# Performance work log

Hardware: AMD Instinct MI355X
Metric: run time of the kernel (lower is better)

Reference implementation:

```python
import jax, jax.numpy as jnp
import numpy as np

NUM_CLASSES = 91
W_CLASS, W_BBOX, W_GIOU = 1.0, 5.0, 2.0


def cxcywh_to_xyxy(b):
    return jnp.concatenate([b[..., :2] - 0.5 * b[..., 2:], b[..., :2] + 0.5 * b[..., 2:]], axis=-1)


def pairwise_giou(b1, b2):
    # b1: [B,Q,4] xyxy, b2: [B,G,4] xyxy -> [B,Q,G]
    area1 = (b1[..., 2] - b1[..., 0]) * (b1[..., 3] - b1[..., 1])
    area2 = (b2[..., 2] - b2[..., 0]) * (b2[..., 3] - b2[..., 1])
    lt = jnp.maximum(b1[:, :, None, :2], b2[:, None, :, :2])
    rb = jnp.minimum(b1[:, :, None, 2:], b2[:, None, :, 2:])
    wh = jnp.clip(rb - lt, 0.0)
    inter = wh[..., 0] * wh[..., 1]
    union = area1[:, :, None] + area2[:, None, :] - inter
    iou = inter / union
    lt2 = jnp.minimum(b1[:, :, None, :2], b2[:, None, :, :2])
    rb2 = jnp.maximum(b1[:, :, None, 2:], b2[:, None, :, 2:])
    wh2 = jnp.clip(rb2 - lt2, 0.0)
    area_c = wh2[..., 0] * wh2[..., 1]
    return iou - (area_c - union) / area_c


def elem_giou(b1, b2):
    # b1, b2: [M,4] xyxy -> [M]
    area1 = (b1[:, 2] - b1[:, 0]) * (b1[:, 3] - b1[:, 1])
    area2 = (b2[:, 2] - b2[:, 0]) * (b2[:, 3] - b2[:, 1])
    lt = jnp.maximum(b1[:, :2], b2[:, :2])
    rb = jnp.minimum(b1[:, 2:], b2[:, 2:])
    wh = jnp.clip(rb - lt, 0.0)
    inter = wh[:, 0] * wh[:, 1]
    union = area1 + area2 - inter
    iou = inter / union
    lt2 = jnp.minimum(b1[:, :2], b2[:, :2])
    rb2 = jnp.maximum(b1[:, 2:], b2[:, 2:])
    wh2 = jnp.clip(rb2 - lt2, 0.0)
    area_c = wh2[:, 0] * wh2[:, 1]
    return iou - (area_c - union) / area_c


def _lsa(cost):
    # Rectangular linear sum assignment (scipy-style shortest augmenting path).
    cost = np.asarray(cost, dtype=np.float64)
    transposed = cost.shape[0] > cost.shape[1]
    if transposed:
        cost = cost.T
    n, m = cost.shape
    u = np.zeros(n)
    v = np.zeros(m)
    path = np.full(m, -1, dtype=np.int64)
    col4row = np.full(n, -1, dtype=np.int64)
    row4col = np.full(m, -1, dtype=np.int64)
    for cur_row in range(n):
        min_val = 0.0
        i = cur_row
        remaining = np.arange(m)
        SR = np.zeros(n, dtype=bool)
        SC = np.zeros(m, dtype=bool)
        shortest = np.full(m, np.inf)
        sink = -1
        while sink == -1:
            SR[i] = True
            r = min_val + cost[i, remaining] - u[i] - v[remaining]
            better = r < shortest[remaining]
            upd = remaining[better]
            shortest[upd] = r[better]
            path[upd] = i
            k = int(np.argmin(shortest[remaining]))
            j = int(remaining[k])
            min_val = shortest[j]
            if not np.isfinite(min_val):
                raise ValueError('infeasible cost matrix')
            if row4col[j] == -1:
                sink = j
            else:
                i = int(row4col[j])
            SC[j] = True
            remaining = np.delete(remaining, k)
        u[cur_row] += min_val
        sr = SR.copy()
        sr[cur_row] = False
        u[sr] += min_val - shortest[col4row[sr]]
        v[SC] -= min_val - shortest[SC]
        j = sink
        while True:
            i = int(path[j])
            row4col[j] = i
            col4row[i], j = j, col4row[i]
            if i == cur_row:
                break
    if transposed:
        a = np.argsort(col4row)
        return col4row[a], a
    return np.arange(n), col4row


def _match(pred_logits, pred_boxes, gt_labels, gt_boxes):
    B, Q, _ = pred_logits.shape
    G = gt_labels.shape[1]
    log_probs = jax.nn.log_softmax(pred_logits, axis=-1)  # [B,Q,C+1]
    labels_c = jnp.clip(gt_labels, 0, NUM_CLASSES)
    cost_class = -jnp.take_along_axis(log_probs, jnp.broadcast_to(labels_c[:, None, :], (B, Q, G)), axis=2)
    cost_bbox = jnp.sum(jnp.abs(pred_boxes[:, :, None, :] - gt_boxes[:, None, :, :]), axis=-1)  # pairwise L1
    cost_giou = -pairwise_giou(cxcywh_to_xyxy(pred_boxes), cxcywh_to_xyxy(gt_boxes))
    C = W_BBOX * cost_bbox + W_CLASS * cost_class + W_GIOU * cost_giou  # [B,Q,G]
    C_np = np.asarray(jax.lax.stop_gradient(C))
    valid = np.asarray(gt_labels) < NUM_CLASSES
    b_idx, s_idx, t_idx = [], [], []
    for i in range(B):  # Hungarian is inherently sequential / host-side (matches torch original)
        cols = np.nonzero(valid[i])[0]
        if cols.size == 0:
            continue
        r, c = _lsa(C_np[i][:, cols])
        b_idx.append(np.full(r.shape, i, dtype=np.int64))
        s_idx.append(r.astype(np.int64))
        t_idx.append(cols[c].astype(np.int64))
    return np.concatenate(b_idx), np.concatenate(s_idx), np.concatenate(t_idx)


def _losses(pred_logits, pred_boxes, gt_boxes, gt_labels, batch_idx, src_idx, tgt_idx):
    B, Q, _ = pred_logits.shape
    log_probs = jax.nn.log_softmax(pred_logits, axis=-1)
    target_classes = jnp.full((B, Q), NUM_CLASSES, dtype=jnp.int32)
    target_classes = target_classes.at[batch_idx, src_idx].set(gt_labels[batch_idx, tgt_idx].astype(jnp.int32))
    nll = -jnp.take_along_axis(log_probs, target_classes[..., None], axis=-1)[..., 0]  # [B,Q]
    empty_weight = jnp.concatenate([jnp.full((NUM_CLASSES,), 0.1, jnp.float32), jnp.ones((1,), jnp.float32)])
    w = empty_weight[target_classes]
    loss_ce = jnp.sum(w * nll) / jnp.sum(w)  # weighted CE, torch 'mean' semantics
    mp = pred_boxes[batch_idx, src_idx][..., :4]
    mg = gt_boxes[batch_idx, tgt_idx]
    loss_bbox = jnp.mean(jnp.abs(mp - mg))
    loss_giou = jnp.mean(1.0 - elem_giou(cxcywh_to_xyxy(mp), cxcywh_to_xyxy(mg)))
    return jnp.stack([loss_ce, loss_bbox, loss_giou])


def setup_inputs() -> dict:
    key = jax.random.key(0)
    k1, k2, k3, k4 = jax.random.split(key, 4)
    B, Q, G = 128, 900, 80
    return {
        'pred_logits': jax.random.normal(k1, (B, Q, NUM_CLASSES + 1), dtype=jnp.float32),
        'pred_boxes': jax.random.uniform(k2, (B, Q, 4), dtype=jnp.float32),
        'gt_labels': jax.random.randint(k3, (B, G), 0, 120, dtype=jnp.int32),
        'gt_boxes': jax.random.uniform(k4, (B, G, 4), dtype=jnp.float32),
    }


def reference(pred_logits, pred_boxes, gt_labels, gt_boxes):
    bi, si, ti = _match(pred_logits, pred_boxes, gt_labels, gt_boxes)
    return _losses(pred_logits, pred_boxes, gt_boxes, gt_labels, bi, si, ti)
```

## Files before the change

kernel.cpp:

```cpp
#include <hip/hip_runtime.h>
#include <math.h>

#define BB 128
#define QQ 900
#define GG 80
#define CC 92
#define NCL 91
#define NSLOT 15

#define COST_OFF 0
#define LSE_OFF  36864000
#define VIDX_OFF 37324800
#define NV_OFF   37365760
#define FPART_OFF 37366272
#define MPART_OFF 37370368

#define FRONT_LDS_BYTES (225 * 93 * 4)

__global__ __launch_bounds__(256) void front_kernel(const float* __restrict__ logits,
                                                    const float* __restrict__ pboxes,
                                                    const float* __restrict__ gboxes,
                                                    const int* __restrict__ glabels,
                                                    float* __restrict__ lse_g,
                                                    int* __restrict__ valid_idx,
                                                    int* __restrict__ nvalid,
                                                    float* __restrict__ cost,
                                                    double* __restrict__ fpart) {
    extern __shared__ float sL[];
    __shared__ int svidx[GG];
    __shared__ int s_n;
    __shared__ int slab[GG];
    __shared__ float sgx0[GG], sgy0[GG], sgx1[GG], sgy1[GG], sgar[GG];
    __shared__ float sgcx[GG], sgcy[GG], sgcz[GG], sgcw[GG];
    __shared__ double sce[4];
    int blk = blockIdx.x;
    int b = blk >> 2;
    int part = blk & 3;
    int tid = threadIdx.x;
    if (tid < 64) {
        int lane = tid;
        bool v0 = glabels[b * GG + lane] < NCL;
        bool v1 = (lane < GG - 64) ? (glabels[b * GG + 64 + lane] < NCL) : false;
        unsigned long long m0 = __ballot(v0);
        unsigned long long m1 = __ballot(v1);
        int c0 = __popcll(m0);
        unsigned long long lower = lane ? (~0ULL >> (64 - lane)) : 0ULL;
        if (v0) { int p = __popcll(m0 & lower); svidx[p] = lane; valid_idx[b * GG + p] = lane; }
        if (v1) { int p = c0 + __popcll(m1 & lower); svidx[p] = 64 + lane; valid_idx[b * GG + p] = 64 + lane; }
        if (lane == 0) { s_n = c0 + __popcll(m1); nvalid[b] = s_n; }
    }
    __syncthreads();
    int n = s_n;

    {
        const float* src = logits + ((size_t)(b * QQ) + part * 225) * CC;
        for (int i = tid; i < 225 * CC; i += 256) {
            int ql = i / CC;
            int c = i - ql * CC;
            sL[ql * 93 + c] = src[i];
        }
    }
    for (int k = tid; k < n; k += 256) {
        int g = svidx[k];
        slab[k] = glabels[b * GG + g];
        float4 gb = ((const float4*)gboxes)[b * GG + g];
        sgcx[k] = gb.x; sgcy[k] = gb.y; sgcz[k] = gb.z; sgcw[k] = gb.w;
        float gx0 = gb.x - 0.5f * gb.z, gy0 = gb.y - 0.5f * gb.w;
        float gx1 = gb.x + 0.5f * gb.z, gy1 = gb.y + 0.5f * gb.w;
        sgx0[k] = gx0; sgy0[k] = gy0; sgx1[k] = gx1; sgy1[k] = gy1;
        sgar[k] = (gx1 - gx0) * (gy1 - gy0);
    }
    __syncthreads();

    int q = part * 225 + tid;
    bool qok = tid < 225;
    const float* row = sL + tid * 93;

    double local = 0.0;
    float lse_q = 0.f;
    if (qok) {
        float mx = -INFINITY;
        for (int c = 0; c < 23; ++c) {
            float x0 = row[4 * c], x1 = row[4 * c + 1], x2 = row[4 * c + 2], x3 = row[4 * c + 3];
            mx = fmaxf(mx, fmaxf(fmaxf(x0, x1), fmaxf(x2, x3)));
        }
        float ssum = 0.f;
        float e91 = 0.f;
        for (int c = 0; c < 23; ++c) {
            float x0 = row[4 * c], x1 = row[4 * c + 1], x2 = row[4 * c + 2], x3 = row[4 * c + 3];
            ssum += expf(x0 - mx) + expf(x1 - mx) + expf(x2 - mx) + expf(x3 - mx);
            if (c == 22) e91 = x3;
        }
        lse_q = mx + logf(ssum);
        lse_g[b * QQ + q] = lse_q;
        local = (double)lse_q - (double)e91;
    }
#pragma unroll
    for (int off = 32; off; off >>= 1) local += __shfl_down(local, off);
    if ((tid & 63) == 0) sce[tid >> 6] = local;

    if (qok) {
        float4 pb = ((const float4*)pboxes)[b * QQ + q];
        float px0 = pb.x - 0.5f * pb.z, py0 = pb.y - 0.5f * pb.w;
        float px1 = pb.x + 0.5f * pb.z, py1 = pb.y + 0.5f * pb.w;
        float parea = (px1 - px0) * (py1 - py0);
        for (int k = 0; k < n; ++k) {
            float l1 = fabsf(pb.x - sgcx[k]) + fabsf(pb.y - sgcy[k]) +
                       fabsf(pb.z - sgcz[k]) + fabsf(pb.w - sgcw[k]);
            float ltx = fmaxf(px0, sgx0[k]), lty = fmaxf(py0, sgy0[k]);
            float rbx = fminf(px1, sgx1[k]), rby = fminf(py1, sgy1[k]);
            float iw = fmaxf(rbx - ltx, 0.f), ih = fmaxf(rby - lty, 0.f);
            float inter = iw * ih;
            float uni = parea + sgar[k] - inter;
            float iou = inter / uni;
            float cx0 = fminf(px0, sgx0[k]), cy0 = fminf(py0, sgy0[k]);
            float cx1 = fmaxf(px1, sgx1[k]), cy1 = fmaxf(py1, sgy1[k]);
            float cw = fmaxf(cx1 - cx0, 0.f), ch = fmaxf(cy1 - cy0, 0.f);
            float ac = cw * ch;
            float giou = iou - (ac - uni) / ac;
            float cls = lse_q - row[slab[k]];
            cost[((size_t)(b * GG + k)) * QQ + q] = 5.f * l1 + cls - 2.f * giou;
        }
    }
    __syncthreads();
    if (tid == 0) fpart[blk] = sce[0] + sce[1] + sce[2] + sce[3];
}

__device__ __forceinline__ unsigned wave_min_u32(unsigned x) {
    unsigned t;
    t = (unsigned)__builtin_amdgcn_update_dpp((int)x, (int)x, 0x111, 0xF, 0xF, false); x = x < t ? x : t;
    t = (unsigned)__builtin_amdgcn_update_dpp((int)x, (int)x, 0x112, 0xF, 0xF, false); x = x < t ? x : t;
    t = (unsigned)__builtin_amdgcn_update_dpp((int)x, (int)x, 0x114, 0xF, 0xF, false); x = x < t ? x : t;
    t = (unsigned)__builtin_amdgcn_update_dpp((int)x, (int)x, 0x118, 0xF, 0xF, false); x = x < t ? x : t;
    t = (unsigned)__builtin_amdgcn_update_dpp((int)x, (int)x, 0x142, 0xF, 0xF, false); x = x < t ? x : t;
    t = (unsigned)__builtin_amdgcn_update_dpp((int)x, (int)x, 0x143, 0xF, 0xF, false); x = x < t ? x : t;
    return (unsigned)__builtin_amdgcn_readlane((int)x, 63);
}
__device__ __forceinline__ float wave_min_f32(float x) {
    float t;
#define MSTEP(ctrl)                                                                               \
    t = __uint_as_float((unsigned)__builtin_amdgcn_update_dpp(                                    \
        (int)__float_as_uint(x), (int)__float_as_uint(x), ctrl, 0xF, 0xF, false));                \
    x = fminf(x, t);
    MSTEP(0x111) MSTEP(0x112) MSTEP(0x114) MSTEP(0x118) MSTEP(0x142) MSTEP(0x143)
#undef MSTEP
    return __uint_as_float((unsigned)__builtin_amdgcn_readlane((int)__float_as_uint(x), 63));
}

__device__ __forceinline__ bool sap_phase(int cur, int lane, const float* cbase,
                                          unsigned valid_mask, float (&v)[NSLOT],
                                          int (&r4c_r)[NSLOT], float (&u_r)[2],
                                          int (&c4r_r)[2]) {
    float sh[NSLOT];
    int path_r[NSLOT];
    float srv_r[2] = {0.f, 0.f};
    unsigned sc = 0, srm = 0;
#pragma unroll
    for (int s = 0; s < NSLOT; ++s) sh[s] = INFINITY;
    int i2 = cur;
    float minv = 0.f;
    int sink = -1;
    for (int pop = 0; pop < QQ && sink < 0; ++pop) {
        float uv = (i2 >> 6) ? u_r[1] : u_r[0];
        float ui = __uint_as_float(
            (unsigned)__builtin_amdgcn_readlane((int)__float_as_uint(uv), i2 & 63));
        const float* crow = cbase + (size_t)i2 * QQ;
        float cv[NSLOT];
#pragma unroll
        for (int s = 0; s < NSLOT; ++s) {
            int j = s * 64 + lane;
            cv[s] = (j < QQ) ? crow[j] : 0.f;
        }
        float base = minv - ui;
        unsigned act = valid_mask & ~sc;
        float lmin = INFINITY;
        int lslot = 0;
#pragma unroll
        for (int s = 0; s < NSLOT; ++s) {
            if ((act >> s) & 1u) {
                float r = base + cv[s] - v[s];
                if (r < sh[s]) { sh[s] = r; path_r[s] = i2; }
                if (sh[s] < lmin) { lmin = sh[s]; lslot = s; }
            }
        }
        float gmin = wave_min_f32(lmin);
        unsigned cand = (lmin == gmin) ? (unsigned)(lslot * 64 + lane) : 0xFFFFFFFFu;
        int lj = (int)wave_min_u32(cand);
        minv = gmin;
        if (lane == (lj & 63)) sc |= (1u << (lj >> 6));
        int rv = -1;
#pragma unroll
        for (int s = 0; s < NSLOT; ++s)
            if (s == (lj >> 6)) rv = r4c_r[s];
        int r4c = __builtin_amdgcn_readlane(rv, lj & 63);
        if (r4c == -1) {
            sink = lj;
        } else {
            i2 = r4c;
            if (lane == (i2 & 63)) {
#pragma unroll
                for (int s = 0; s < 2; ++s)
                    if (s == (i2 >> 6)) { srm |= (1u << s); srv_r[s] = minv; }
            }
        }
    }
    if (sink < 0) return false;
    if (lane == (cur & 63)) {
#pragma unroll
        for (int s = 0; s < 2; ++s)
            if (s == (cur >> 6)) u_r[s] += minv;
    }
#pragma unroll
    for (int s = 0; s < 2; ++s)
        if ((srm >> s) & 1u) u_r[s] += minv - srv_r[s];
#pragma unroll
    for (int s = 0; s < NSLOT; ++s)
        if ((sc >> s) & 1u) v[s] -= (minv - sh[s]);
    int j = sink;
    while (true) {
        int pslot = j >> 6, plane = j & 63;
        int pv = 0;
#pragma unroll
        for (int s = 0; s < NSLOT; ++s)
            if (s == pslot) pv = path_r[s];
        int pi = __builtin_amdgcn_readlane(pv, plane);
        if (lane == plane) {
#pragma unroll
            for (int s = 0; s < NSLOT; ++s)
                if (s == pslot) r4c_r[s] = pi;
        }
        int cslot = pi >> 6, clane = pi & 63;
        int cvv = 0;
#pragma unroll
        for (int s = 0; s < 2; ++s)
            if (s == cslot) cvv = c4r_r[s];
        int nj = __builtin_amdgcn_readlane(cvv, clane);
        if (lane == clane) {
#pragma unroll
            for (int s = 0; s < 2; ++s)
                if (s == cslot) c4r_r[s] = j;
        }
        j = nj;
        if (pi == cur) break;
    }
    return true;
}

__global__ __launch_bounds__(64, 1) void lsa_kernel(const float* __restrict__ cost,
                                                    const int* __restrict__ nvalid,
                                                    const int* __restrict__ valid_idx,
                                                    const int* __restrict__ glabels,
                                                    const float* __restrict__ lse_g,
                                                    const float* __restrict__ pboxes,
                                                    const float* __restrict__ gboxes,
                                                    const float* __restrict__ logits,
                                                    double* __restrict__ mpart) {
    int b = blockIdx.x;
    int n = nvalid[b];
    const float* cbase = cost + (size_t)b * GG * QQ;
    int lane = threadIdx.x;

    float v[NSLOT];
    int r4c_r[NSLOT];
    float u_r[2];
    int c4r_r[2];
    unsigned valid_mask = 0x3FFFu | ((lane < QQ - 14 * 64) ? 0x4000u : 0u);
#pragma unroll
    for (int s = 0; s < NSLOT; ++s) { v[s] = 0.f; r4c_r[s] = -1; }
#pragma unroll
    for (int s = 0; s < 2; ++s) { u_r[s] = 0.f; c4r_r[s] = -1; }

    for (int cur = 0; cur < n; ++cur)
        sap_phase(cur, lane, cbase, valid_mask, v, r4c_r, u_r, c4r_r);

    double ce = 0.0, dl1 = 0.0, dgi = 0.0;
#pragma unroll
    for (int s = 0; s < 2; ++s) {
        int r = s * 64 + lane;
        int q = c4r_r[s];
        if (r < n && q >= 0 && q < QQ) {
            int g = valid_idx[b * GG + r];
            int label = glabels[b * GG + g];
            if (label < 0 || label >= CC) label = 0;
            size_t ro = ((size_t)b * QQ + q) * CC;
            float ls = lse_g[b * QQ + q];
            float nll_lab = ls - logits[ro + label];
            float nll_no = ls - logits[ro + NCL];
            ce += 0.1 * (double)nll_lab - (double)nll_no;
            float4 pb = ((const float4*)pboxes)[b * QQ + q];
            float4 gb = ((const float4*)gboxes)[b * GG + g];
            float l1 = fabsf(pb.x - gb.x) + fabsf(pb.y - gb.y) + fabsf(pb.z - gb.z) + fabsf(pb.w - gb.w);
            float px0 = pb.x - 0.5f * pb.z, py0 = pb.y - 0.5f * pb.w;
            float px1 = pb.x + 0.5f * pb.z, py1 = pb.y + 0.5f * pb.w;
            float gx0 = gb.x - 0.5f * gb.z, gy0 = gb.y - 0.5f * gb.w;
            float gx1 = gb.x + 0.5f * gb.z, gy1 = gb.y + 0.5f * gb.w;
            float parea = (px1 - px0) * (py1 - py0);
            float garea = (gx1 - gx0) * (gy1 - gy0);
            float ltx = fmaxf(px0, gx0), lty = fmaxf(py0, gy0);
            float rbx = fminf(px1, gx1), rby = fminf(py1, gy1);
            float iw = fmaxf(rbx - ltx, 0.f), ih = fmaxf(rby - lty, 0.f);
            float inter = iw * ih;
            float uni = parea + garea - inter;
            float iou = inter / uni;
            float cx0 = fminf(px0, gx0), cy0 = fminf(py0, gy0);
            float cx1 = fmaxf(px1, gx1), cy1 = fmaxf(py1, gy1);
            float cw = fmaxf(cx1 - cx0, 0.f), ch = fmaxf(cy1 - cy0, 0.f);
            float ac = cw * ch;
            float giou = iou - (ac - uni) / ac;
            dl1 += (double)l1;
            dgi += 1.0 - (double)giou;
        }
    }
#pragma unroll
    for (int off = 32; off; off >>= 1) {
        ce += __shfl_down(ce, off);
        dl1 += __shfl_down(dl1, off);
        dgi += __shfl_down(dgi, off);
    }
    if (lane == 0) {
        mpart[b * 3 + 0] = ce;
        mpart[b * 3 + 1] = dl1;
        mpart[b * 3 + 2] = dgi;
    }
}

__global__ __launch_bounds__(64) void final_kernel(const int* __restrict__ nvalid,
                                                   const double* __restrict__ fpart,
                                                   const double* __restrict__ mpart,
                                                   float* __restrict__ out) {
    int lane = threadIdx.x;
    int m = nvalid[lane] + nvalid[64 + lane];
    double fb = 0.0;
    for (int i = lane; i < BB * 4; i += 64) fb += fpart[i];
    double ce = 0.0, dl1 = 0.0, dgi = 0.0;
#pragma unroll
    for (int s = 0; s < 2; ++s) {
        int bb = s * 64 + lane;
        ce += mpart[bb * 3 + 0];
        dl1 += mpart[bb * 3 + 1];
        dgi += mpart[bb * 3 + 2];
    }
#pragma unroll
    for (int off = 32; off; off >>= 1) {
        m += __shfl_down(m, off);
        fb += __shfl_down(fb, off);
        ce += __shfl_down(ce, off);
        dl1 += __shfl_down(dl1, off);
        dgi += __shfl_down(dgi, off);
    }
    if (lane == 0) {
        double M = (double)m;
        double sum_w = (double)(BB * QQ) - 0.9 * M;
        out[0] = (float)((fb + ce) / sum_w);
        out[1] = (float)(dl1 / (4.0 * M));
        out[2] = (float)(dgi / M);
    }
}

extern "C" void kernel_launch(void* const* d_in, const int* in_sizes, int n_in,
                              void* d_out, int out_size, void* d_ws, size_t ws_size,
                              hipStream_t stream) {
    const float* logits = (const float*)d_in[0];
    const float* pboxes = (const float*)d_in[1];
    const int* glabels = (const int*)d_in[2];
    const float* gboxes = (const float*)d_in[3];
    float* out = (float*)d_out;

    char* ws = (char*)d_ws;
    float* cost = (float*)(ws + COST_OFF);
    float* lse = (float*)(ws + LSE_OFF);
    int* vidx = (int*)(ws + VIDX_OFF);
    int* nval = (int*)(ws + NV_OFF);
    double* fpart = (double*)(ws + FPART_OFF);
    double* mpart = (double*)(ws + MPART_OFF);

    (void)hipFuncSetAttribute((const void*)front_kernel,
                              hipFuncAttributeMaxDynamicSharedMemorySize, FRONT_LDS_BYTES);

    front_kernel<<<BB * 4, 256, FRONT_LDS_BYTES, stream>>>(logits, pboxes, gboxes, glabels, lse,
                                                           vidx, nval, cost, fpart);
    lsa_kernel<<<BB, 64, 0, stream>>>(cost, nval, vidx, glabels, lse, pboxes, gboxes, logits, mpart);
    final_kernel<<<1, 64, 0, stream>>>(nval, fpart, mpart, out);
}
```

Baseline: 247.7 us.

## Cache cost rows in LDS for LSA and split front kernel into smaller blocks

The LSA kernel now copies the first 44 cost rows for its batch into LDS (about 158 KB) and reads those rows from LDS during the shortest-augmenting-path loop, using global memory only for later rows. This targets the latency of repeated global/L2 row loads in the serial Hungarian loop. The front kernel is re-partitioned into 8 blocks of 128 threads per batch instead of 4 blocks of 256, and its partial sums are now stored as float instead of double. Risks include the up-front copy cost, lower occupancy from the large LDS allocation, and slight precision loss in the partial sums.

Result: slower. 290.2 us (+17.2%).

```diff
diff --git a/kernel.cpp b/kernel.cpp
--- a/kernel.cpp
+++ b/kernel.cpp
@@ -8,6 +8,9 @@
 #define NCL 91
 #define NSLOT 15
 
+#define NPART 8
+#define QPB 128
+
 #define COST_OFF 0
 #define LSE_OFF  36864000
 #define VIDX_OFF 37324800
@@ -15,9 +18,11 @@
 #define FPART_OFF 37366272
 #define MPART_OFF 37370368
 
-#define FRONT_LDS_BYTES (225 * 93 * 4)
-
-__global__ __launch_bounds__(256) void front_kernel(const float* __restrict__ logits,
+#define FRONT_LDS_BYTES (QPB * 93 * 4)
+#define NCACHE 44
+#define LSA_LDS_BYTES (NCACHE * QQ * 4)
+
+__global__ __launch_bounds__(128) void front_kernel(const float* __restrict__ logits,
                                                     const float* __restrict__ pboxes,
                                                     const float* __restrict__ gboxes,
                                                     const int* __restrict__ glabels,
@@ -25,18 +30,21 @@
                                                     int* __restrict__ valid_idx,
                                                     int* __restrict__ nvalid,
                                                     float* __restrict__ cost,
-                                                    double* __restrict__ fpart) {
+                                                    float* __restrict__ fpart) {
     extern __shared__ float sL[];
     __shared__ int svidx[GG];
     __shared__ int s_n;
     __shared__ int slab[GG];
     __shared__ float sgx0[GG], sgy0[GG], sgx1[GG], sgy1[GG], sgar[GG];
     __shared__ float sgcx[GG], sgcy[GG], sgcz[GG], sgcw[GG];
-    __shared__ double sce[4];
+    __shared__ double sce[2];
     int blk = blockIdx.x;
-    int b = blk >> 2;
-    int part = blk & 3;
+    int b = blk >> 3;
+    int part = blk & 7;
     int tid = threadIdx.x;
+    int q0 = part * QPB;
+    int qcnt = QQ - q0;
+    if (qcnt > QPB) qcnt = QPB;
     if (tid < 64) {
         int lane = tid;
         bool v0 = glabels[b * GG + lane] < NCL;
@@ -53,14 +61,14 @@
     int n = s_n;
 
     {
-        const float* src = logits + ((size_t)(b * QQ) + part * 225) * CC;
-        for (int i = tid; i < 225 * CC; i += 256) {
+        const float* src = logits + ((size_t)b * QQ + q0) * CC;
+        for (int i = tid; i < qcnt * CC; i += 128) {
             int ql = i / CC;
             int c = i - ql * CC;
             sL[ql * 93 + c] = src[i];
         }
     }
-    for (int k = tid; k < n; k += 256) {
+    for (int k = tid; k < n; k += 128) {
         int g = svidx[k];
         slab[k] = glabels[b * GG + g];
         float4 gb = ((const float4*)gboxes)[b * GG + g];
@@ -72,8 +80,8 @@
     }
     __syncthreads();
 
-    int q = part * 225 + tid;
-    bool qok = tid < 225;
+    int q = q0 + tid;
+    bool qok = tid < qcnt;
     const float* row = sL + tid * 93;
 
     double local = 0.0;
@@ -123,7 +131,7 @@
         }
     }
     __syncthreads();
-    if (tid == 0) fpart[blk] = sce[0] + sce[1] + sce[2] + sce[3];
+    if (tid == 0) fpart[blk] = (float)(sce[0] + sce[1]);
 }
 
 __device__ __forceinline__ unsigned wave_min_u32(unsigned x) {
@@ -148,6 +156,7 @@
 }
 
 __device__ __forceinline__ bool sap_phase(int cur, int lane, const float* cbase,
+                                          const float* sC, int ncache,
                                           unsigned valid_mask, float (&v)[NSLOT],
                                           int (&r4c_r)[NSLOT], float (&u_r)[2],
                                           int (&c4r_r)[2]) {
@@ -164,12 +173,21 @@
         float uv = (i2 >> 6) ? u_r[1] : u_r[0];
         float ui = __uint_as_float(
             (unsigned)__builtin_amdgcn_readlane((int)__float_as_uint(uv), i2 & 63));
-        const float* crow = cbase + (size_t)i2 * QQ;
         float cv[NSLOT];
-#pragma unroll
-        for (int s = 0; s < NSLOT; ++s) {
-            int j = s * 64 + lane;
-            cv[s] = (j < QQ) ? crow[j] : 0.f;
+        if (i2 < ncache) {
+            const float* srow = sC + i2 * QQ;
+#pragma unroll
+            for (int s = 0; s < NSLOT; ++s) {
+                int j = s * 64 + lane;
+                cv[s] = (j < QQ) ? srow[j] : 0.f;
+            }
+        } else {
+            const float* crow = cbase + (size_t)i2 * QQ;
+#pragma unroll
+            for (int s = 0; s < NSLOT; ++s) {
+                int j = s * 64 + lane;
+                cv[s] = (j < QQ) ? crow[j] : 0.f;
+            }
         }
         float base = minv - ui;
         unsigned act = valid_mask & ~sc;
@@ -255,10 +273,20 @@
                                                     const float* __restrict__ gboxes,
                                                     const float* __restrict__ logits,
                                                     double* __restrict__ mpart) {
+    extern __shared__ float sC[];
     int b = blockIdx.x;
     int n = nvalid[b];
     const float* cbase = cost + (size_t)b * GG * QQ;
     int lane = threadIdx.x;
+
+    int ncache = n < NCACHE ? n : NCACHE;
+    {
+        const float4* s4 = (const float4*)cbase;
+        float4* d4 = (float4*)sC;
+        int cnt = ncache * (QQ / 4);
+        for (int i = lane; i < cnt; i += 64) d4[i] = s4[i];
+    }
+    __syncthreads();
 
     float v[NSLOT];
     int r4c_r[NSLOT];
@@ -271,7 +299,7 @@
     for (int s = 0; s < 2; ++s) { u_r[s] = 0.f; c4r_r[s] = -1; }
 
     for (int cur = 0; cur < n; ++cur)
-        sap_phase(cur, lane, cbase, valid_mask, v, r4c_r, u_r, c4r_r);
+        sap_phase(cur, lane, cbase, sC, ncache, valid_mask, v, r4c_r, u_r, c4r_r);
 
     double ce = 0.0, dl1 = 0.0, dgi = 0.0;
 #pragma unroll
@@ -325,13 +353,13 @@
 }
 
 __global__ __launch_bounds__(64) void final_kernel(const int* __restrict__ nvalid,
-                                                   const double* __restrict__ fpart,
+                                                   const float* __restrict__ fpart,
                                                    const double* __restrict__ mpart,
                                                    float* __restrict__ out) {
     int lane = threadIdx.x;
     int m = nvalid[lane] + nvalid[64 + lane];
     double fb = 0.0;
-    for (int i = lane; i < BB * 4; i += 64) fb += fpart[i];
+    for (int i = lane; i < BB * NPART; i += 64) fb += (double)fpart[i];
     double ce = 0.0, dl1 = 0.0, dgi = 0.0;
 #pragma unroll
     for (int s = 0; s < 2; ++s) {
@@ -371,14 +399,17 @@
     float* lse = (float*)(ws + LSE_OFF);
     int* vidx = (int*)(ws + VIDX_OFF);
     int* nval = (int*)(ws + NV_OFF);
-    double* fpart = (double*)(ws + FPART_OFF);
+    float* fpart = (float*)(ws + FPART_OFF);
     double* mpart = (double*)(ws + MPART_OFF);
 
     (void)hipFuncSetAttribute((const void*)front_kernel,
                               hipFuncAttributeMaxDynamicSharedMemorySize, FRONT_LDS_BYTES);
-
-    front_kernel<<<BB * 4, 256, FRONT_LDS_BYTES, stream>>>(logits, pboxes, gboxes, glabels, lse,
-                                                           vidx, nval, cost, fpart);
-    lsa_kernel<<<BB, 64, 0, stream>>>(cost, nval, vidx, glabels, lse, pboxes, gboxes, logits, mpart);
+    (void)hipFuncSetAttribute((const void*)lsa_kernel,
+                              hipFuncAttributeMaxDynamicSharedMemorySize, LSA_LDS_BYTES);
+
+    front_kernel<<<BB * NPART, 128, FRONT_LDS_BYTES, stream>>>(logits, pboxes, gboxes, glabels,
+                                                               lse, vidx, nval, cost, fpart);
+    lsa_kernel<<<BB, 64, LSA_LDS_BYTES, stream>>>(cost, nval, vidx, glabels, lse, pboxes, gboxes,
+                                                  logits, mpart);
     final_kernel<<<1, 64, 0, stream>>>(nval, fpart, mpart, out);
 }
```
